# Optimization experiments

Measured on AMD Instinct MI355X. Metric: run time of the kernel, lower is better.

The kernel has to match this reference:

```python
import jax, jax.numpy as jnp
import numpy as np

N = 50000
E = 800000
DIN = 256
DH = 256
DOUT = 256
R = 8
B = 4


def setup_inputs() -> dict:
    key = jax.random.key(0)
    ks = jax.random.split(key, 12)
    s = 0.05
    return {
        "x": jax.random.normal(ks[0], (N, DIN), jnp.float32),
        "edge_index": jax.random.randint(ks[1], (2, E), 0, N, jnp.int64),
        "edge_type": jax.random.randint(ks[2], (E,), 0, R, jnp.int64),
        "basis1": jax.random.normal(ks[3], (B, DIN, DH), jnp.float32) * s,
        "comp1": jax.random.normal(ks[4], (R, B), jnp.float32) * s,
        "root1": jax.random.normal(ks[5], (DIN, DH), jnp.float32) * s,
        "bias1": jnp.zeros((DH,), jnp.float32),
        "basis2": jax.random.normal(ks[6], (B, DH, DOUT), jnp.float32) * s,
        "comp2": jax.random.normal(ks[7], (R, B), jnp.float32) * s,
        "root2": jax.random.normal(ks[8], (DH, DOUT), jnp.float32) * s,
        "bias2": jnp.zeros((DOUT,), jnp.float32),
    }


def rgcn_conv(x, src, dst, edge_type, basis, comp, root, bias):
    # Basis-decomposed relational conv (PyG RGCNConv, aggr='mean').
    # xb: per-node transform by each basis matrix -> [N, B, out]
    xb = jnp.einsum('ni,bio->nbo', x, basis)
    # Per-edge message: mix bases with relation coefficients -> [E, out]
    msg = jnp.einsum('eb,ebo->eo', comp[edge_type], xb[src])
    # Mean aggregation per (dst, relation): divide each edge by the count of
    # edges of its relation arriving at its destination, then scatter-add.
    key = dst * R + edge_type
    cnt = jax.ops.segment_sum(jnp.ones((msg.shape[0],), x.dtype), key,
                              num_segments=x.shape[0] * R)
    norm = 1.0 / jnp.maximum(cnt, 1.0)
    agg = jax.ops.segment_sum(msg * norm[key][:, None], dst,
                              num_segments=x.shape[0])
    return agg + x @ root + bias


def reference(x, edge_index, edge_type, basis1, comp1, root1, bias1,
              basis2, comp2, root2, bias2):
    src, dst = edge_index[0], edge_index[1]
    h = rgcn_conv(x, src, dst, edge_type, basis1, comp1, root1, bias1)
    h = jax.nn.relu(h)
    # dropout(p=0.4) is identity in eval mode
    out = rgcn_conv(h, src, dst, edge_type, basis2, comp2, root2, bias2)
    return out
```

## Files before the change

### kernel.cpp

```cpp
#include <hip/hip_runtime.h>
#include <hip/hip_bf16.h>

constexpr int N_NODES = 50000;
constexpr int N_EDGES = 800000;
constexpr int R_REL   = 8;
constexpr int BASES   = 4;
constexpr int D       = 256;
constexpr int KZ      = BASES * D;
constexpr int KT      = KZ + D;
constexpr int WSTRIDE = 16;
constexpr int DUMMY_P = 8 << 20;

constexpr int EB  = (N_EDGES + 255) / 256;
constexpr int EB4 = (N_EDGES + 1023) / 1024;
constexpr int NB  = (N_NODES + 255) / 256;
constexpr int CB4 = (N_NODES * 128) / 1024;
constexpr int WKB = KT / 64;
constexpr int WB  = (N_NODES * WSTRIDE) / 256;
constexpr int CAP = N_EDGES + N_NODES * 8;
constexpr int FB4 = (CAP + 1023) / 1024;

typedef __attribute__((ext_vector_type(8))) short bf16x8;
typedef __attribute__((ext_vector_type(4))) float f32x4;

__device__ inline float bfu_lo(unsigned u) { return __uint_as_float(u << 16); }
__device__ inline float bfu_hi(unsigned u) { return __uint_as_float(u & 0xFFFF0000u); }
__device__ inline unsigned short f2bu(float f) {
  __hip_bfloat16 h = __float2bfloat16(f);
  return *reinterpret_cast<unsigned short*>(&h);
}
__device__ inline void store_out(float* p, float v) { *p = v; }
__device__ inline void store_out(__hip_bfloat16* p, float v) { *p = __float2bfloat16(v); }

__device__ inline void gload_lds16(void* lds, const void* g) {
  __builtin_amdgcn_global_load_lds(
      (const __attribute__((address_space(1))) unsigned*)g,
      (__attribute__((address_space(3))) unsigned*)lds, 16, 0, 0);
}

__global__ __launch_bounds__(256) void prep_kernel(
    const int* __restrict__ ei, const int* __restrict__ et,
    int* __restrict__ cnt,
    const float* __restrict__ x, unsigned* __restrict__ x2,
    const float* __restrict__ basis1, const float* __restrict__ root1,
    __hip_bfloat16* __restrict__ WT1,
    const float* __restrict__ basis2, const float* __restrict__ root2,
    __hip_bfloat16* __restrict__ WT2,
    int* __restrict__ packed) {
  __shared__ __hip_bfloat16 tile[16][256];
  int bid = blockIdx.x;
  int tid = threadIdx.x;

  if (bid < EB4) {
    int e4 = (bid * 256 + tid) * 4;
    if (e4 < N_EDGES) {
      int4 dv = *(const int4*)(ei + N_EDGES + e4);
      int4 tv = *(const int4*)(et + e4);
      atomicAdd(&cnt[dv.x * R_REL + tv.x], 1);
      atomicAdd(&cnt[dv.y * R_REL + tv.y], 1);
      atomicAdd(&cnt[dv.z * R_REL + tv.z], 1);
      atomicAdd(&cnt[dv.w * R_REL + tv.w], 1);
    }
    return;
  }
  bid -= EB4;
  if (bid < CB4) {
    int idx = (bid * 256 + tid) * 4;
    const float* px = x + (size_t)idx * 2;
    float4 a = *(const float4*)(px);
    float4 b = *(const float4*)(px + 4);
    uint4 o;
    o.x = (unsigned)f2bu(a.x) | ((unsigned)f2bu(a.y) << 16);
    o.y = (unsigned)f2bu(a.z) | ((unsigned)f2bu(a.w) << 16);
    o.z = (unsigned)f2bu(b.x) | ((unsigned)f2bu(b.y) << 16);
    o.w = (unsigned)f2bu(b.z) | ((unsigned)f2bu(b.w) << 16);
    *(uint4*)(x2 + idx) = o;
    return;
  }
  bid -= CB4;
  if (bid < 2 * WKB) {
    const float* basis = (bid < WKB) ? basis1 : basis2;
    const float* root  = (bid < WKB) ? root1 : root2;
    __hip_bfloat16* WT = (bid < WKB) ? WT1 : WT2;
    int wb = (bid < WKB) ? bid : bid - WKB;
    int k0 = wb * 64;
#pragma unroll
    for (int pass = 0; pass < 4; pass++) {
      int kp = k0 + pass * 16;
#pragma unroll
      for (int r = 0; r < 16; r++) {
        int k = kp + r;
        const float* srow = (k < KZ)
            ? basis + ((size_t)(k & 3) * D + (k >> 2)) * D
            : root + (size_t)(k - KZ) * D;
        tile[r][tid] = __float2bfloat16(srow[tid]);
      }
      __syncthreads();
      __hip_bfloat16* dst = WT + (size_t)tid * KT + kp;
#pragma unroll
      for (int c = 0; c < 2; c++) {
        union { short s[8]; int4 v; } u;
#pragma unroll
        for (int r = 0; r < 8; r++)
          u.s[r] = *reinterpret_cast<short*>(&tile[c * 8 + r][tid]);
        *(int4*)(dst + c * 8) = u.v;
      }
      __syncthreads();
    }
    return;
  }
  bid -= 2 * WKB;
  {
    int i = (bid * 256 + tid) * 4;
    if (i < CAP) {
      int4 f = make_int4(DUMMY_P, DUMMY_P, DUMMY_P, DUMMY_P);
      *(int4*)(packed + i) = f;
    }
  }
}

__global__ __launch_bounds__(256) void scanA_winv_kernel(
    const int* __restrict__ cnt, int* __restrict__ bsum,
    const float* __restrict__ comp1, float4* __restrict__ wtab1,
    const float* __restrict__ comp2, float4* __restrict__ wtab2) {
  __shared__ int sd[256];
  int bid = blockIdx.x;
  int tid = threadIdx.x;
  if (bid < NB) {
    int n = bid * 256 + tid;
    int d = 0;
    if (n < N_NODES) {
#pragma unroll
      for (int r = 0; r < R_REL; r++) d += cnt[n * R_REL + r];
      d = (d + 7) & ~7;
    }
    sd[tid] = d;
    __syncthreads();
    for (int off = 128; off > 0; off >>= 1) {
      if (tid < off) sd[tid] += sd[tid + off];
      __syncthreads();
    }
    if (tid == 0) bsum[bid] = sd[0];
    return;
  }
  bid -= NB;
  {
    const float* comp = (bid < WB) ? comp1 : comp2;
    float4* wtab = (bid < WB) ? wtab1 : wtab2;
    int lb = (bid < WB) ? bid : bid - WB;
    int idx = lb * 256 + tid;
    int r = idx & (WSTRIDE - 1);
    int n = idx >> 4;
    float4 w = make_float4(0.f, 0.f, 0.f, 0.f);
    if (r < R_REL) {
      int c = cnt[n * R_REL + r];
      float inv = 1.0f / (float)(c > 0 ? c : 1);
      w.x = comp[r * BASES + 0] * inv;
      w.y = comp[r * BASES + 1] * inv;
      w.z = comp[r * BASES + 2] * inv;
      w.w = comp[r * BASES + 3] * inv;
    }
    wtab[idx] = w;
  }
}

__global__ __launch_bounds__(256) void scan_phaseB(
    const int* __restrict__ bsum, int* __restrict__ boff,
    int* __restrict__ estart) {
  __shared__ int sd[256];
  int tid = threadIdx.x;
  int v = (tid < NB) ? bsum[tid] : 0;
  sd[tid] = v;
  __syncthreads();
  for (int off = 1; off < 256; off <<= 1) {
    int t = (tid >= off) ? sd[tid - off] : 0;
    __syncthreads();
    sd[tid] += t;
    __syncthreads();
  }
  if (tid < NB) boff[tid] = sd[tid] - v;
  if (tid == NB - 1) estart[N_NODES] = sd[tid];
}

__global__ __launch_bounds__(256) void scan_phaseC(
    const int* __restrict__ cnt, const int* __restrict__ boff,
    int* __restrict__ estart, int* __restrict__ cursor) {
  __shared__ int sd[256];
  int tid = threadIdx.x;
  int n = blockIdx.x * 256 + tid;
  int d = 0;
  if (n < N_NODES) {
#pragma unroll
    for (int r = 0; r < R_REL; r++) d += cnt[n * R_REL + r];
    d = (d + 7) & ~7;
  }
  sd[tid] = d;
  __syncthreads();
  for (int off = 1; off < 256; off <<= 1) {
    int t = (tid >= off) ? sd[tid - off] : 0;
    __syncthreads();
    sd[tid] += t;
    __syncthreads();
  }
  if (n < N_NODES) {
    estart[n] = boff[blockIdx.x] + sd[tid] - d;
    cursor[n] = 0;
  }
}

__global__ __launch_bounds__(256) void bucket_kernel(
    const int* __restrict__ ei, const int* __restrict__ et,
    const int* __restrict__ estart, int* __restrict__ cursor,
    int* __restrict__ packed) {
  int e = blockIdx.x * 256 + threadIdx.x;
  if (e < N_EDGES) {
    int src = ei[e];
    int dst = ei[N_EDGES + e];
    int rt  = et[e];
    int pos = estart[dst] + atomicAdd(&cursor[dst], 1);
    packed[pos] = src | (rt << 20);
  }
}

__device__ inline float2 pfma(float s, float2 a, float2 c) {
  c.x = fmaf(s, a.x, c.x);
  c.y = fmaf(s, a.y, c.y);
  return c;
}

__device__ inline void edge_fma(float2 acc[BASES][2], uint2 v, float4 w) {
  float2 a01 = make_float2(bfu_lo(v.x), bfu_hi(v.x));
  float2 a23 = make_float2(bfu_lo(v.y), bfu_hi(v.y));
  acc[0][0] = pfma(w.x, a01, acc[0][0]); acc[0][1] = pfma(w.x, a23, acc[0][1]);
  acc[1][0] = pfma(w.y, a01, acc[1][0]); acc[1][1] = pfma(w.y, a23, acc[1][1]);
  acc[2][0] = pfma(w.z, a01, acc[2][0]); acc[2][1] = pfma(w.z, a23, acc[2][1]);
  acc[3][0] = pfma(w.w, a01, acc[3][0]); acc[3][1] = pfma(w.w, a23, acc[3][1]);
}

__global__ __launch_bounds__(256) void aggregate_kernel(
    const unsigned* __restrict__ x2,
    const int* __restrict__ packed,
    const int* __restrict__ estart,
    const float4* __restrict__ wtab,
    __hip_bfloat16* __restrict__ zA)
{
  int tid = threadIdx.x;
  int lane = tid & 63;
  int n = __builtin_amdgcn_readfirstlane(blockIdx.x * 4 + (tid >> 6));
  int s = __builtin_amdgcn_readfirstlane(estart[n]);
  int e = __builtin_amdgcn_readfirstlane(estart[n + 1]);
  const int voff = lane * 2;
  const float4* wt = wtab + (size_t)n * WSTRIDE;

  float2 acc[BASES][2] = {};

  for (int base = s; base < e; base += 8) {
    int4 q0 = *(const int4*)(packed + base);
    int4 q1 = *(const int4*)(packed + base + 4);
    int p0 = __builtin_amdgcn_readfirstlane(q0.x);
    int p1 = __builtin_amdgcn_readfirstlane(q0.y);
    int p2 = __builtin_amdgcn_readfirstlane(q0.z);
    int p3 = __builtin_amdgcn_readfirstlane(q0.w);
    int p4 = __builtin_amdgcn_readfirstlane(q1.x);
    int p5 = __builtin_amdgcn_readfirstlane(q1.y);
    int p6 = __builtin_amdgcn_readfirstlane(q1.z);
    int p7 = __builtin_amdgcn_readfirstlane(q1.w);
    const unsigned* r0 = x2 + ((size_t)(p0 & 0xFFFFF) << 7);
    const unsigned* r1 = x2 + ((size_t)(p1 & 0xFFFFF) << 7);
    const unsigned* r2 = x2 + ((size_t)(p2 & 0xFFFFF) << 7);
    const unsigned* r3 = x2 + ((size_t)(p3 & 0xFFFFF) << 7);
    const unsigned* r4 = x2 + ((size_t)(p4 & 0xFFFFF) << 7);
    const unsigned* r5 = x2 + ((size_t)(p5 & 0xFFFFF) << 7);
    const unsigned* r6 = x2 + ((size_t)(p6 & 0xFFFFF) << 7);
    const unsigned* r7 = x2 + ((size_t)(p7 & 0xFFFFF) << 7);
    uint2 v0 = *(const uint2*)(r0 + voff);
    uint2 v1 = *(const uint2*)(r1 + voff);
    uint2 v2 = *(const uint2*)(r2 + voff);
    uint2 v3 = *(const uint2*)(r3 + voff);
    uint2 v4 = *(const uint2*)(r4 + voff);
    uint2 v5 = *(const uint2*)(r5 + voff);
    uint2 v6 = *(const uint2*)(r6 + voff);
    uint2 v7 = *(const uint2*)(r7 + voff);
    float4 w0 = wt[p0 >> 20];
    float4 w1 = wt[p1 >> 20];
    float4 w2 = wt[p2 >> 20];
    float4 w3 = wt[p3 >> 20];
    float4 w4 = wt[p4 >> 20];
    float4 w5 = wt[p5 >> 20];
    float4 w6 = wt[p6 >> 20];
    float4 w7 = wt[p7 >> 20];
    edge_fma(acc, v0, w0);
    edge_fma(acc, v1, w1);
    edge_fma(acc, v2, w2);
    edge_fma(acc, v3, w3);
    edge_fma(acc, v4, w4);
    edge_fma(acc, v5, w5);
    edge_fma(acc, v6, w6);
    edge_fma(acc, v7, w7);
  }

  union { short s[8]; int4 v; } u0, u1;
#pragma unroll
  for (int b = 0; b < BASES; b++) {
    u0.s[b]     = (short)f2bu(acc[b][0].x);
    u0.s[4 + b] = (short)f2bu(acc[b][0].y);
    u1.s[b]     = (short)f2bu(acc[b][1].x);
    u1.s[4 + b] = (short)f2bu(acc[b][1].y);
  }
  __hip_bfloat16* zrow = zA + (size_t)n * KZ;
  *(int4*)(zrow + 16 * lane) = u0.v;
  *(int4*)(zrow + 16 * lane + 8) = u1.v;
}

#define BM 128
#define BN 256
#define BK 32

template <bool RELU, typename OutT>
__global__ __launch_bounds__(512) void gemm_kernel(
    const __hip_bfloat16* __restrict__ Az,
    const __hip_bfloat16* __restrict__ Aself,
    const __hip_bfloat16* __restrict__ Bt,
    const float* __restrict__ bias, OutT* __restrict__ C, int M) {
  __shared__ __align__(16) __hip_bfloat16 As[BM * BK];
  __shared__ __align__(16) __hip_bfloat16 Bs[BN * BK];
  int tid = threadIdx.x;
  int m0 = blockIdx.x * BM;
  int wave = tid >> 6, lane = tid & 63;
  int wm = wave & 1, wn = wave >> 1;
  int l15 = lane & 15, quad = lane >> 4;

  int colS = (lane & 3) * 8;
  int rowA = wave * 16 + (lane >> 2);
  int grA  = min(m0 + rowA, M - 1);
  const __hip_bfloat16* gAz = Az + (size_t)grA * KZ + colS;
  const __hip_bfloat16* gAs = Aself + (size_t)grA * D + colS;
  const __hip_bfloat16* gB0 = Bt + (size_t)(wave * 32 + (lane >> 2)) * KT + colS;
  const __hip_bfloat16* gB1 = gB0 + 16 * KT;
  __hip_bfloat16* lA  = As + wave * 512;
  __hip_bfloat16* lB0 = Bs + wave * 1024;
  __hip_bfloat16* lB1 = Bs + wave * 1024 + 512;

  f32x4 acc[4][4] = {};

  for (int k0 = 0; k0 < KT; k0 += BK) {
    const __hip_bfloat16* srcA = (k0 < KZ) ? (gAz + k0) : (gAs + (k0 - KZ));
    gload_lds16(lA, srcA);
    gload_lds16(lB0, gB0 + k0);
    gload_lds16(lB1, gB1 + k0);
    __syncthreads();

    bf16x8 af[4], bfr[4];
#pragma unroll
    for (int mt = 0; mt < 4; mt++)
      af[mt] = *(const bf16x8*)(As + (wm * 64 + mt * 16 + l15) * BK + quad * 8);
#pragma unroll
    for (int nt = 0; nt < 4; nt++)
      bfr[nt] = *(const bf16x8*)(Bs + (wn * 64 + nt * 16 + l15) * BK + quad * 8);
#pragma unroll
    for (int mt = 0; mt < 4; mt++)
#pragma unroll
      for (int nt = 0; nt < 4; nt++)
        acc[mt][nt] = __builtin_amdgcn_mfma_f32_16x16x32_bf16(
            af[mt], bfr[nt], acc[mt][nt], 0, 0, 0);
    __syncthreads();
  }

#pragma unroll
  for (int nt = 0; nt < 4; nt++) {
    int cg = wn * 64 + nt * 16 + l15;
    float bv = bias[cg];
#pragma unroll
    for (int mt = 0; mt < 4; mt++) {
#pragma unroll
      for (int r = 0; r < 4; r++) {
        int rg = m0 + wm * 64 + mt * 16 + quad * 4 + r;
        if (rg < M) {
          float v = acc[mt][nt][r] + bv;
          if (RELU) v = fmaxf(v, 0.f);
          store_out(C + (size_t)rg * D + cg, v);
        }
      }
    }
  }
}

static inline char* carve(char*& p, size_t bytes) {
  char* r = p;
  p += (bytes + 255) & ~(size_t)255;
  return r;
}

extern "C" void kernel_launch(void* const* d_in, const int* in_sizes, int n_in,
                              void* d_out, int out_size, void* d_ws,
                              size_t ws_size, hipStream_t stream) {
  const float* x      = (const float*)d_in[0];
  const int*   ei     = (const int*)d_in[1];
  const int*   et     = (const int*)d_in[2];
  const float* basis1 = (const float*)d_in[3];
  const float* comp1  = (const float*)d_in[4];
  const float* root1  = (const float*)d_in[5];
  const float* bias1  = (const float*)d_in[6];
  const float* basis2 = (const float*)d_in[7];
  const float* comp2  = (const float*)d_in[8];
  const float* root2  = (const float*)d_in[9];
  const float* bias2  = (const float*)d_in[10];
  float* out = (float*)d_out;

  char* ws = (char*)d_ws;
  int* cnt    = (int*)carve(ws, (size_t)N_NODES * R_REL * 4);
  int* estart = (int*)carve(ws, (size_t)(N_NODES + 1) * 4);
  int* cursor = (int*)carve(ws, (size_t)N_NODES * 4);
  int* bsum   = (int*)carve(ws, 256 * 4);
  int* boff   = (int*)carve(ws, 256 * 4);
  int* packed = (int*)carve(ws, (size_t)CAP * 4);
  float4* wtab1 = (float4*)carve(ws, (size_t)N_NODES * WSTRIDE * 16);
  float4* wtab2 = (float4*)carve(ws, (size_t)N_NODES * WSTRIDE * 16);
  __hip_bfloat16* WT1 = (__hip_bfloat16*)carve(ws, (size_t)D * KT * 2);
  __hip_bfloat16* WT2 = (__hip_bfloat16*)carve(ws, (size_t)D * KT * 2);
  unsigned* xb = (unsigned*)carve(ws, (size_t)N_NODES * D * 2);
  __hip_bfloat16* h = (__hip_bfloat16*)carve(ws, (size_t)N_NODES * D * 2);
  __hip_bfloat16* zA = (__hip_bfloat16*)carve(ws, (size_t)N_NODES * KZ * 2);

  hipMemsetAsync(cnt, 0, (size_t)N_NODES * R_REL * 4, stream);

  prep_kernel<<<EB4 + CB4 + 2 * WKB + FB4, 256, 0, stream>>>(
      ei, et, cnt, x, xb, basis1, root1, WT1, basis2, root2, WT2, packed);
  scanA_winv_kernel<<<NB + 2 * WB, 256, 0, stream>>>(cnt, bsum, comp1, wtab1,
                                                     comp2, wtab2);
  scan_phaseB<<<1, 256, 0, stream>>>(bsum, boff, estart);
  scan_phaseC<<<NB, 256, 0, stream>>>(cnt, boff, estart, cursor);
  bucket_kernel<<<EB, 256, 0, stream>>>(ei, et, estart, cursor, packed);

  dim3 ggrid((N_NODES + BM - 1) / BM, 1);
  const int AB = (N_NODES + 3) / 4;

  aggregate_kernel<<<AB, 256, 0, stream>>>(xb, packed, estart, wtab1, zA);
  gemm_kernel<true, __hip_bfloat16><<<ggrid, 512, 0, stream>>>(
      zA, (const __hip_bfloat16*)xb, WT1, bias1, h, N_NODES);

  aggregate_kernel<<<AB, 256, 0, stream>>>((const unsigned*)h, packed, estart,
                                           wtab2, zA);
  gemm_kernel<false, float><<<ggrid, 512, 0, stream>>>(
      zA, h, WT2, bias2, out, N_NODES);
}
```

Measured before the change: 482.8 us.

## Replace global-atomic CSR bucketing with two-pass coarse/fine radix sort by destination

Builds the destination-sorted edge list with a two-level radix partition instead of per-edge global atomics: coarse bins of 256 nodes are histogrammed and scattered using LDS atomics, then each bin is fine-sorted per node in LDS while the per-(node, relation) counts and the padded prefix offsets are computed locally. This removes the 800K global atomic increments on cnt and cursor and the scattered packed writes, at the cost of an extra pass over the edges, a temporary coarse buffer and more small kernel launches. The coarse packing stores src in 16 bits, which assumes node ids below 65536.

After: 443.9 us. 1.09x faster.

```diff
diff --git a/kernel.cpp b/kernel.cpp
--- a/kernel.cpp
+++ b/kernel.cpp
@@ -11,8 +11,10 @@
 constexpr int WSTRIDE = 16;
 constexpr int DUMMY_P = 8 << 20;
 
-constexpr int EB  = (N_EDGES + 255) / 256;
-constexpr int EB4 = (N_EDGES + 1023) / 1024;
+constexpr int NHI    = (N_NODES + 255) / 256;
+constexpr int NS_BLK = 200;
+constexpr int CH     = N_EDGES / NS_BLK;
+
 constexpr int NB  = (N_NODES + 255) / 256;
 constexpr int CB4 = (N_NODES * 128) / 1024;
 constexpr int WKB = KT / 64;
@@ -40,7 +42,7 @@
 
 __global__ __launch_bounds__(256) void prep_kernel(
     const int* __restrict__ ei, const int* __restrict__ et,
-    int* __restrict__ cnt,
+    int* __restrict__ gcoarse,
     const float* __restrict__ x, unsigned* __restrict__ x2,
     const float* __restrict__ basis1, const float* __restrict__ root1,
     __hip_bfloat16* __restrict__ WT1,
@@ -48,22 +50,23 @@
     __hip_bfloat16* __restrict__ WT2,
     int* __restrict__ packed) {
   __shared__ __hip_bfloat16 tile[16][256];
+  __shared__ int hist[NHI];
   int bid = blockIdx.x;
   int tid = threadIdx.x;
 
-  if (bid < EB4) {
-    int e4 = (bid * 256 + tid) * 4;
-    if (e4 < N_EDGES) {
-      int4 dv = *(const int4*)(ei + N_EDGES + e4);
-      int4 tv = *(const int4*)(et + e4);
-      atomicAdd(&cnt[dv.x * R_REL + tv.x], 1);
-      atomicAdd(&cnt[dv.y * R_REL + tv.y], 1);
-      atomicAdd(&cnt[dv.z * R_REL + tv.z], 1);
-      atomicAdd(&cnt[dv.w * R_REL + tv.w], 1);
+  if (bid < NS_BLK) {
+    if (tid < NHI) hist[tid] = 0;
+    __syncthreads();
+    int start = bid * CH, end = start + CH;
+    for (int i = start + tid; i < end; i += 256) {
+      int dst = ei[N_EDGES + i];
+      atomicAdd(&hist[dst >> 8], 1);
     }
+    __syncthreads();
+    if (tid < NHI && hist[tid] > 0) atomicAdd(&gcoarse[tid], hist[tid]);
     return;
   }
-  bid -= EB4;
+  bid -= NS_BLK;
   if (bid < CB4) {
     int idx = (bid * 256 + tid) * 4;
     const float* px = x + (size_t)idx * 2;
@@ -119,28 +122,121 @@
   }
 }
 
-__global__ __launch_bounds__(256) void scanA_winv_kernel(
-    const int* __restrict__ cnt, int* __restrict__ bsum,
+__global__ __launch_bounds__(256) void coarse_prefix_kernel(
+    const int* __restrict__ gcoarse, int* __restrict__ gbase,
+    int* __restrict__ gcur) {
+  __shared__ int sd[256];
+  int tid = threadIdx.x;
+  int v = (tid < NHI) ? gcoarse[tid] : 0;
+  sd[tid] = v;
+  __syncthreads();
+  for (int off = 1; off < 256; off <<= 1) {
+    int t = (tid >= off) ? sd[tid - off] : 0;
+    __syncthreads();
+    sd[tid] += t;
+    __syncthreads();
+  }
+  if (tid < NHI) {
+    int b = sd[tid] - v;
+    gbase[tid] = b;
+    gcur[tid] = b;
+  }
+}
+
+__global__ __launch_bounds__(256) void coarse_scatter_kernel(
+    const int* __restrict__ ei, const int* __restrict__ et,
+    int* __restrict__ gcur, int* __restrict__ coarse) {
+  __shared__ int hist[NHI];
+  __shared__ int lbase[NHI];
+  __shared__ int lcnt[NHI];
+  int bid = blockIdx.x;
+  int tid = threadIdx.x;
+  if (tid < NHI) { hist[tid] = 0; lcnt[tid] = 0; }
+  __syncthreads();
+  int start = bid * CH, end = start + CH;
+  for (int i = start + tid; i < end; i += 256)
+    atomicAdd(&hist[ei[N_EDGES + i] >> 8], 1);
+  __syncthreads();
+  if (tid < NHI) lbase[tid] = atomicAdd(&gcur[tid], hist[tid]);
+  __syncthreads();
+  for (int i = start + tid; i < end; i += 256) {
+    int src = ei[i];
+    int dst = ei[N_EDGES + i];
+    int rt  = et[i];
+    int bin = dst >> 8;
+    int rank = atomicAdd(&lcnt[bin], 1);
+    coarse[lbase[bin] + rank] = src | (rt << 16) | ((dst & 255) << 19);
+  }
+}
+
+__global__ __launch_bounds__(256) void fine_hist_kernel(
+    const int* __restrict__ coarse, const int* __restrict__ gbase,
+    const int* __restrict__ gcoarse, int* __restrict__ cnt,
+    int* __restrict__ lestart, int* __restrict__ btot) {
+  __shared__ int c2[256 * R_REL];
+  __shared__ int sd[256];
+  int b = blockIdx.x;
+  int tid = threadIdx.x;
+#pragma unroll
+  for (int k = tid; k < 256 * R_REL; k += 256) c2[k] = 0;
+  __syncthreads();
+  int base = gbase[b], n_e = gcoarse[b];
+  for (int i = tid; i < n_e; i += 256) {
+    int e = coarse[base + i];
+    int key = ((e >> 19) & 255) * R_REL + ((e >> 16) & 7);
+    atomicAdd(&c2[key], 1);
+  }
+  __syncthreads();
+  int nodebase = b * 256;
+#pragma unroll
+  for (int k = tid; k < 256 * R_REL; k += 256) {
+    int n = nodebase + (k >> 3);
+    if (n < N_NODES) cnt[n * R_REL + (k & 7)] = c2[k];
+  }
+  int d = 0;
+#pragma unroll
+  for (int r = 0; r < R_REL; r++) d += c2[tid * R_REL + r];
+  int dp = (d + 7) & ~7;
+  sd[tid] = dp;
+  __syncthreads();
+  for (int off = 1; off < 256; off <<= 1) {
+    int t = (tid >= off) ? sd[tid - off] : 0;
+    __syncthreads();
+    sd[tid] += t;
+    __syncthreads();
+  }
+  lestart[b * 256 + tid] = sd[tid] - dp;
+  if (tid == 255) btot[b] = sd[255];
+}
+
+__global__ __launch_bounds__(256) void btot_prefix_kernel(
+    const int* __restrict__ btot, int* __restrict__ bbase,
+    int* __restrict__ estart) {
+  __shared__ int sd[256];
+  int tid = threadIdx.x;
+  int v = (tid < NHI) ? btot[tid] : 0;
+  sd[tid] = v;
+  __syncthreads();
+  for (int off = 1; off < 256; off <<= 1) {
+    int t = (tid >= off) ? sd[tid - off] : 0;
+    __syncthreads();
+    sd[tid] += t;
+    __syncthreads();
+  }
+  if (tid < NHI) bbase[tid] = sd[tid] - v;
+  if (tid == NHI - 1) estart[N_NODES] = sd[tid];
+}
+
+__global__ __launch_bounds__(256) void finalize_kernel(
+    const int* __restrict__ bbase, const int* __restrict__ lestart,
+    int* __restrict__ estart, const int* __restrict__ cnt,
     const float* __restrict__ comp1, float4* __restrict__ wtab1,
     const float* __restrict__ comp2, float4* __restrict__ wtab2) {
-  __shared__ int sd[256];
   int bid = blockIdx.x;
   int tid = threadIdx.x;
   if (bid < NB) {
     int n = bid * 256 + tid;
-    int d = 0;
-    if (n < N_NODES) {
-#pragma unroll
-      for (int r = 0; r < R_REL; r++) d += cnt[n * R_REL + r];
-      d = (d + 7) & ~7;
-    }
-    sd[tid] = d;
-    __syncthreads();
-    for (int off = 128; off > 0; off >>= 1) {
-      if (tid < off) sd[tid] += sd[tid + off];
-      __syncthreads();
-    }
-    if (tid == 0) bsum[bid] = sd[0];
+    if (n < N_NODES) estart[n] = bbase[n >> 8] + lestart[n];
     return;
   }
   bid -= NB;
@@ -164,61 +260,24 @@
   }
 }
 
-__global__ __launch_bounds__(256) void scan_phaseB(
-    const int* __restrict__ bsum, int* __restrict__ boff,
-    int* __restrict__ estart) {
-  __shared__ int sd[256];
-  int tid = threadIdx.x;
-  int v = (tid < NB) ? bsum[tid] : 0;
-  sd[tid] = v;
-  __syncthreads();
-  for (int off = 1; off < 256; off <<= 1) {
-    int t = (tid >= off) ? sd[tid - off] : 0;
-    __syncthreads();
-    sd[tid] += t;
-    __syncthreads();
-  }
-  if (tid < NB) boff[tid] = sd[tid] - v;
-  if (tid == NB - 1) estart[N_NODES] = sd[tid];
-}
-
-__global__ __launch_bounds__(256) void scan_phaseC(
-    const int* __restrict__ cnt, const int* __restrict__ boff,
-    int* __restrict__ estart, int* __restrict__ cursor) {
-  __shared__ int sd[256];
-  int tid = threadIdx.x;
-  int n = blockIdx.x * 256 + tid;
-  int d = 0;
-  if (n < N_NODES) {
-#pragma unroll
-    for (int r = 0; r < R_REL; r++) d += cnt[n * R_REL + r];
-    d = (d + 7) & ~7;
-  }
-  sd[tid] = d;
-  __syncthreads();
-  for (int off = 1; off < 256; off <<= 1) {
-    int t = (tid >= off) ? sd[tid - off] : 0;
-    __syncthreads();
-    sd[tid] += t;
-    __syncthreads();
-  }
-  if (n < N_NODES) {
-    estart[n] = boff[blockIdx.x] + sd[tid] - d;
-    cursor[n] = 0;
-  }
-}
-
-__global__ __launch_bounds__(256) void bucket_kernel(
-    const int* __restrict__ ei, const int* __restrict__ et,
-    const int* __restrict__ estart, int* __restrict__ cursor,
-    int* __restrict__ packed) {
-  int e = blockIdx.x * 256 + threadIdx.x;
-  if (e < N_EDGES) {
-    int src = ei[e];
-    int dst = ei[N_EDGES + e];
-    int rt  = et[e];
-    int pos = estart[dst] + atomicAdd(&cursor[dst], 1);
-    packed[pos] = src | (rt << 20);
+__global__ __launch_bounds__(256) void fine_scatter_kernel(
+    const int* __restrict__ coarse, const int* __restrict__ gbase,
+    const int* __restrict__ gcoarse, const int* __restrict__ bbase,
+    const int* __restrict__ lestart, int* __restrict__ packed) {
+  __shared__ int lest[256];
+  __shared__ int lcur[256];
+  int b = blockIdx.x;
+  int tid = threadIdx.x;
+  lest[tid] = lestart[b * 256 + tid];
+  lcur[tid] = 0;
+  __syncthreads();
+  int base = gbase[b], n_e = gcoarse[b];
+  int sb = bbase[b];
+  for (int i = tid; i < n_e; i += 256) {
+    int e = coarse[base + i];
+    int lo = (e >> 19) & 255;
+    int rank = atomicAdd(&lcur[lo], 1);
+    packed[sb + lest[lo] + rank] = (e & 0xFFFF) | (((e >> 16) & 7) << 20);
   }
 }
 
@@ -408,12 +467,16 @@
   float* out = (float*)d_out;
 
   char* ws = (char*)d_ws;
-  int* cnt    = (int*)carve(ws, (size_t)N_NODES * R_REL * 4);
-  int* estart = (int*)carve(ws, (size_t)(N_NODES + 1) * 4);
-  int* cursor = (int*)carve(ws, (size_t)N_NODES * 4);
-  int* bsum   = (int*)carve(ws, 256 * 4);
-  int* boff   = (int*)carve(ws, 256 * 4);
-  int* packed = (int*)carve(ws, (size_t)CAP * 4);
+  int* cnt     = (int*)carve(ws, (size_t)N_NODES * R_REL * 4);
+  int* estart  = (int*)carve(ws, (size_t)(N_NODES + 1) * 4);
+  int* coarse  = (int*)carve(ws, (size_t)N_EDGES * 4);
+  int* lestart = (int*)carve(ws, (size_t)NHI * 256 * 4);
+  int* gcoarse = (int*)carve(ws, 256 * 4);
+  int* gbase   = (int*)carve(ws, 256 * 4);
+  int* gcur    = (int*)carve(ws, 256 * 4);
+  int* btot    = (int*)carve(ws, 256 * 4);
+  int* bbase   = (int*)carve(ws, 256 * 4);
+  int* packed  = (int*)carve(ws, (size_t)CAP * 4);
   float4* wtab1 = (float4*)carve(ws, (size_t)N_NODES * WSTRIDE * 16);
   float4* wtab2 = (float4*)carve(ws, (size_t)N_NODES * WSTRIDE * 16);
   __hip_bfloat16* WT1 = (__hip_bfloat16*)carve(ws, (size_t)D * KT * 2);
@@ -422,15 +485,19 @@
   __hip_bfloat16* h = (__hip_bfloat16*)carve(ws, (size_t)N_NODES * D * 2);
   __hip_bfloat16* zA = (__hip_bfloat16*)carve(ws, (size_t)N_NODES * KZ * 2);
 
-  hipMemsetAsync(cnt, 0, (size_t)N_NODES * R_REL * 4, stream);
-
-  prep_kernel<<<EB4 + CB4 + 2 * WKB + FB4, 256, 0, stream>>>(
-      ei, et, cnt, x, xb, basis1, root1, WT1, basis2, root2, WT2, packed);
-  scanA_winv_kernel<<<NB + 2 * WB, 256, 0, stream>>>(cnt, bsum, comp1, wtab1,
-                                                     comp2, wtab2);
-  scan_phaseB<<<1, 256, 0, stream>>>(bsum, boff, estart);
-  scan_phaseC<<<NB, 256, 0, stream>>>(cnt, boff, estart, cursor);
-  bucket_kernel<<<EB, 256, 0, stream>>>(ei, et, estart, cursor, packed);
+  hipMemsetAsync(gcoarse, 0, 256 * 4, stream);
+
+  prep_kernel<<<NS_BLK + CB4 + 2 * WKB + FB4, 256, 0, stream>>>(
+      ei, et, gcoarse, x, xb, basis1, root1, WT1, basis2, root2, WT2, packed);
+  coarse_prefix_kernel<<<1, 256, 0, stream>>>(gcoarse, gbase, gcur);
+  coarse_scatter_kernel<<<NS_BLK, 256, 0, stream>>>(ei, et, gcur, coarse);
+  fine_hist_kernel<<<NHI, 256, 0, stream>>>(coarse, gbase, gcoarse, cnt,
+                                            lestart, btot);
+  btot_prefix_kernel<<<1, 256, 0, stream>>>(btot, bbase, estart);
+  finalize_kernel<<<NB + 2 * WB, 256, 0, stream>>>(bbase, lestart, estart, cnt,
+                                                   comp1, wtab1, comp2, wtab2);
+  fine_scatter_kernel<<<NHI, 256, 0, stream>>>(coarse, gbase, gcoarse, bbase,
+                                               lestart, packed);
 
   dim3 ggrid((N_NODES + BM - 1) / BM, 1);
   const int AB = (N_NODES + 3) / 4;
```
